# Optimization experiments

Hardware: AMD Instinct MI355X
Metric: run time of the kernel (lower is better)

Reference implementation:

```python
import jax, jax.numpy as jnp
import numpy as np

RES = 14
N = RES * RES
NH = 8
KD = 32
D = 128   # attn_ratio * key_dim
DH = 1024 # D * NH
DIM = 384
B = 128
SCALE = KD ** -0.5


def _bias_idxs():
    pts = [(i, j) for i in range(RES) for j in range(RES)]
    offs, idxs = {}, []
    for p1 in pts:
        for p2 in pts:
            o = (abs(p1[0] - p2[0]), abs(p1[1] - p2[1]))
            offs.setdefault(o, len(offs))
            idxs.append(offs[o])
    return np.array(idxs, np.int32).reshape(N, N), len(offs)

BIAS_IDXS, NUM_OFF = _bias_idxs()  # (N, N), 196 distinct |offset| pairs


def setup_inputs() -> dict:
    key = jax.random.key(0)
    ks = jax.random.split(key, 32)
    g = lambda i, shape, s=0.05: jax.random.normal(ks[i], shape, jnp.float32) * s
    pos = lambda i, shape: jax.random.uniform(ks[i], shape, jnp.float32, minval=0.5, maxval=1.5)
    return dict(
        x=jax.random.normal(ks[0], (B, DIM, RES, RES), jnp.float32),
        qw=g(1, (NH * KD, DIM)), qb=g(2, (NH * KD,)), q_s=pos(3, (NH * KD,)), q_t=g(4, (NH * KD,)),
        kw=g(5, (NH * KD, DIM)), kb=g(6, (NH * KD,)), k_s=pos(7, (NH * KD,)), k_t=g(8, (NH * KD,)),
        vw=g(9, (DH, DIM)), vb=g(10, (DH,)), v_s=pos(11, (DH,)), v_t=g(12, (DH,)),
        lvw=g(13, (DH, 3, 3)), lvb=g(14, (DH,)), lv_s=pos(15, (DH,)), lv_t=g(16, (DH,)),
        th1w=g(17, (NH, NH), 0.3), th1b=g(18, (NH,)),
        th2w=g(19, (NH, NH), 0.3), th2b=g(20, (NH,)),
        ab=g(21, (NH, NUM_OFF)),
        pw=g(22, (DIM, DH)), pb=g(23, (DIM,)), p_s=pos(24, (DIM,)), p_t=g(25, (DIM,)),
    )


def _c(v):
    return v[None, :, None, None]


def conv1x1_bn(x, w, b, s, t):
    # 1x1 conv (NCHW) + eval-mode BN folded to per-channel affine
    y = jnp.einsum('bchw,oc->bohw', x, w) + _c(b)
    return y * _c(s) + _c(t)


def reference(x, qw, qb, q_s, q_t, kw, kb, k_s, k_t, vw, vb, v_s, v_t,
              lvw, lvb, lv_s, lv_t, th1w, th1b, th2w, th2b, ab,
              pw, pb, p_s, p_t):
    Bb = x.shape[0]
    # q,k: (B, NH, N, KD)
    q = conv1x1_bn(x, qw, qb, q_s, q_t).reshape(Bb, NH, KD, N).transpose(0, 1, 3, 2)
    k = conv1x1_bn(x, kw, kb, k_s, k_t).reshape(Bb, NH, KD, N).transpose(0, 1, 3, 2)
    v4 = conv1x1_bn(x, vw, vb, v_s, v_t)  # (B, DH, RES, RES)
    # local depthwise 3x3 conv + BN on v
    vl = jax.lax.conv_general_dilated(
        v4, lvw.reshape(DH, 1, 3, 3), window_strides=(1, 1), padding='SAME',
        dimension_numbers=('NCHW', 'OIHW', 'NCHW'), feature_group_count=DH)
    vl = (vl + _c(lvb)) * _c(lv_s) + _c(lv_t)
    v = v4.reshape(Bb, NH, D, N).transpose(0, 1, 3, 2)  # (B, NH, N, D)

    attn = jnp.einsum('bhid,bhjd->bhij', q, k) * SCALE
    attn = attn + ab[:, BIAS_IDXS][None]  # relative-position bias (1, NH, N, N)
    attn = jnp.einsum('bhij,gh->bgij', attn, th1w) + _c(th1b)  # talking head 1
    attn = jax.nn.softmax(attn, axis=-1)
    attn = jnp.einsum('bhij,gh->bgij', attn, th2w) + _c(th2b)  # talking head 2

    o = jnp.einsum('bhij,bhjd->bhid', attn, v)  # (B, NH, N, D)
    o = o.transpose(0, 1, 3, 2).reshape(Bb, DH, RES, RES) + vl
    o = jax.nn.relu(o)
    return conv1x1_bn(o, pw, pb, p_s, p_t)
```

## Files before the change

### kernel.cpp

```cpp
#include <hip/hip_runtime.h>
#include <hip/hip_bf16.h>
#include <stdint.h>

typedef __hip_bfloat16 bf16;
typedef short short4v __attribute__((ext_vector_type(4)));
typedef short short8 __attribute__((ext_vector_type(8)));
typedef float f32x4 __attribute__((ext_vector_type(4)));
typedef float f32x16 __attribute__((ext_vector_type(16)));

#define NB 128
#define NPIX 196
#define NPAD 208
#define VP 208
#define QROWS 208
#define NH 8
#define KD 32
#define DHEAD 128
#define DH 1024
#define DIM 384
#define SCALE 0.17677669529663687f

__device__ __forceinline__ float b2f(bf16 v) { return __bfloat162float(v); }
__device__ __forceinline__ bf16 f2b(float f) { return __float2bfloat16(f); }
__device__ __forceinline__ float us2f(unsigned short u) {
  union { unsigned int i; float f; } v; v.i = (unsigned int)u << 16; return v.f;
}
__device__ __forceinline__ short f2us(float f) {
  bf16 b = __float2bfloat16(f);
  return *(short*)&b;
}

__device__ __forceinline__ void gll16(const void* g, void* l) {
  auto gp = reinterpret_cast<const uint32_t __attribute__((address_space(1)))*>(
      reinterpret_cast<uintptr_t>(g));
  auto lp = reinterpret_cast<uint32_t __attribute__((address_space(3)))*>(
      reinterpret_cast<uintptr_t>(l));
  __builtin_amdgcn_global_load_lds(gp, lp, 16, 0, 0);
}

__global__ __launch_bounds__(256) void k_cvt4(const float* __restrict__ s0,
                                              const float* __restrict__ s1,
                                              const float* __restrict__ s2,
                                              const float* __restrict__ s3,
                                              bf16* __restrict__ dst,
                                              const float* __restrict__ th1w,
                                              const float* __restrict__ th1b,
                                              const float* __restrict__ ab,
                                              float* __restrict__ ab2g,
                                              float* __restrict__ c1g) {
  if (blockIdx.x >= 3840) {
    int t = threadIdx.x;
    for (int pos = t; pos < NH * NPIX; pos += 256) {
      int g = pos / NPIX, off = pos - g * NPIX;
      float s = th1b[g];
#pragma unroll
      for (int h = 0; h < 8; ++h)
        s += th1w[g * 8 + h] * ab[h * NPIX + off];
      ab2g[pos] = s;
    }
    if (t < 64) c1g[t] = th1w[t] * SCALE;
    return;
  }
  int i = blockIdx.x * 256 + threadIdx.x;
  const float* src; int o;
  if (i < 98304)       { src = s0; o = i; }
  else if (i < 196608) { src = s1; o = i - 98304; }
  else if (i < 589824) { src = s2; o = i - 196608; }
  else                 { src = s3; o = i - 589824; }
  dst[i] = f2b(src[o]);
}

__global__ __launch_bounds__(256) void k_xt(const float* __restrict__ x,
                                            bf16* __restrict__ XT) {
  __shared__ bf16 tile[32][33];
  int ct = blockIdx.x, nt = blockIdx.y, b = blockIdx.z;
  int c0 = ct * 32, n0 = nt * 32;
  int tc = threadIdx.x >> 5, tn = threadIdx.x & 31;
#pragma unroll
  for (int r = 0; r < 4; ++r) {
    int c = tc + r * 8;
    int n = n0 + tn;
    float v = 0.f;
    if (n < NPIX) v = x[((size_t)b * DIM + c0 + c) * NPIX + n];
    tile[c][tn] = f2b(v);
  }
  __syncthreads();
#pragma unroll
  for (int r = 0; r < 4; ++r) {
    int n = n0 + tc + r * 8;
    if (n < NPAD) XT[((size_t)b * NPAD + n) * DIM + c0 + tn] = tile[tn][tc + r * 8];
  }
}

__global__ __launch_bounds__(256, 2) void k_qkv2(
    const bf16* __restrict__ Wf, const bf16* __restrict__ XT,
    const float* __restrict__ qb, const float* __restrict__ qs, const float* __restrict__ qt,
    const float* __restrict__ kb, const float* __restrict__ ks, const float* __restrict__ kt,
    const float* __restrict__ vb, const float* __restrict__ vs, const float* __restrict__ vt,
    bf16* __restrict__ qf, bf16* __restrict__ kf, bf16* __restrict__ v4) {
  __shared__ __align__(16) char lds[2][32768];
  const int NWG = 12 * 208;
  int id = blockIdx.x;
  int id2 = (id & 7) * (NWG >> 3) + (id >> 3);
  int mt = id2 % 12, nt = id2 / 12;
  int m0 = mt * 128, n0 = nt * 128;
  int tid = threadIdx.x, lane = tid & 63;
  int wv = tid >> 6, wm = wv >> 1, wn = wv & 1;

  f32x4 acc[4][4];
#pragma unroll
  for (int mi = 0; mi < 4; ++mi)
#pragma unroll
    for (int ni = 0; ni < 4; ++ni)
#pragma unroll
      for (int r = 0; r < 4; ++r) acc[mi][ni][r] = 0.f;

  auto stage = [&](int buf, int t) {
    int k0 = t * 64;
#pragma unroll
    for (int j = 0; j < 4; ++j) {
      int gi = tid + j * 256;
      int row = gi >> 3, g = gi & 7;
      int sk = k0 + ((g ^ (row & 7)) << 3);
      gll16(Wf + (size_t)(m0 + row) * DIM + sk, &lds[buf][gi * 16]);
      gll16(XT + (size_t)(n0 + row) * DIM + sk, &lds[buf][16384 + gi * 16]);
    }
  };
  auto compute = [&](int buf) {
    const char* Ab = lds[buf];
    const char* Bb = lds[buf] + 16384;
    int kq = lane >> 4, il = lane & 15;
#pragma unroll
    for (int ksb = 0; ksb < 2; ++ksb) {
      int G = ksb * 4 + kq;
      short8 af[4], bfr[4];
#pragma unroll
      for (int mi = 0; mi < 4; ++mi) {
        int row = wm * 64 + mi * 16 + il;
        af[mi] = *(const short8*)(Ab + row * 128 + ((G ^ (row & 7)) << 4));
      }
#pragma unroll
      for (int ni = 0; ni < 4; ++ni) {
        int row = wn * 64 + ni * 16 + il;
        bfr[ni] = *(const short8*)(Bb + row * 128 + ((G ^ (row & 7)) << 4));
      }
#pragma unroll
      for (int mi = 0; mi < 4; ++mi)
#pragma unroll
        for (int ni = 0; ni < 4; ++ni)
          acc[mi][ni] = __builtin_amdgcn_mfma_f32_16x16x32_bf16(af[mi], bfr[ni], acc[mi][ni], 0, 0, 0);
    }
  };

  stage(0, 0);
  __syncthreads();
  for (int t = 0; t < 6; ++t) {
    if (t < 5) stage((t + 1) & 1, t + 1);
    compute(t & 1);
    __syncthreads();
  }

  int cq = lane >> 4, cn = lane & 15;
#pragma unroll
  for (int mi = 0; mi < 4; ++mi) {
    int mbase = m0 + wm * 64 + mi * 16;
    const float *bp, *sp, *tp;
    int segbase, segid;
    if (mbase < 256)      { bp = qb; sp = qs; tp = qt; segbase = 0;   segid = 0; }
    else if (mbase < 512) { bp = kb; sp = ks; tp = kt; segbase = 256; segid = 1; }
    else                  { bp = vb; sp = vs; tp = vt; segbase = 512; segid = 2; }
#pragma unroll
    for (int r = 0; r < 4; ++r) {
      int ms = mbase - segbase + cq * 4 + r;
      float bi = bp[ms], sc = sp[ms], tt = tp[ms];
#pragma unroll
      for (int ni = 0; ni < 4; ++ni) {
        int n = n0 + wn * 64 + ni * 16 + cn;
        int b = n / NPAD;
        int nn = n - b * NPAD;
        float y = (acc[mi][ni][r] + bi) * sc + tt;
        y = (nn < NPIX) ? y : 0.f;
        if (segid == 2) {
          v4[((size_t)b * DH + ms) * VP + nn] = f2b(y);
        } else {
          bf16* dst = segid ? kf : qf;
          dst[(((size_t)b * NH + (ms >> 5)) * QROWS + nn) * KD + (ms & 31)] = f2b(y);
        }
      }
    }
  }
}

__global__ __launch_bounds__(256, 2) void k_p2(
    const bf16* __restrict__ Pw, const bf16* __restrict__ OT,
    const float* __restrict__ pb, const float* __restrict__ ps, const float* __restrict__ pt,
    float* __restrict__ out) {
  __shared__ __align__(16) char lds[2][32768];
  const int NWG = 3 * 208;
  int id = blockIdx.x;
  int id2 = (id & 7) * (NWG >> 3) + (id >> 3);
  int mt = id2 % 3, nt = id2 / 3;
  int m0 = mt * 128, n0 = nt * 128;
  int tid = threadIdx.x, lane = tid & 63;
  int wv = tid >> 6, wm = wv >> 1, wn = wv & 1;

  f32x4 acc[4][4];
#pragma unroll
  for (int mi = 0; mi < 4; ++mi)
#pragma unroll
    for (int ni = 0; ni < 4; ++ni)
#pragma unroll
      for (int r = 0; r < 4; ++r) acc[mi][ni][r] = 0.f;

  auto stage = [&](int buf, int t) {
    int k0 = t * 64;
#pragma unroll
    for (int j = 0; j < 4; ++j) {
      int gi = tid + j * 256;
      int row = gi >> 3, g = gi & 7;
      int sk = k0 + ((g ^ (row & 7)) << 3);
      gll16(Pw + (size_t)(m0 + row) * DH + sk, &lds[buf][gi * 16]);
      gll16(OT + (size_t)(n0 + row) * DH + sk, &lds[buf][16384 + gi * 16]);
    }
  };
  auto compute = [&](int buf) {
    const char* Ab = lds[buf];
    const char* Bb = lds[buf] + 16384;
    int kq = lane >> 4, il = lane & 15;
#pragma unroll
    for (int ksb = 0; ksb < 2; ++ksb) {
      int G = ksb * 4 + kq;
      short8 af[4], bfr[4];
#pragma unroll
      for (int mi = 0; mi < 4; ++mi) {
        int row = wm * 64 + mi * 16 + il;
        af[mi] = *(const short8*)(Ab + row * 128 + ((G ^ (row & 7)) << 4));
      }
#pragma unroll
      for (int ni = 0; ni < 4; ++ni) {
        int row = wn * 64 + ni * 16 + il;
        bfr[ni] = *(const short8*)(Bb + row * 128 + ((G ^ (row & 7)) << 4));
      }
#pragma unroll
      for (int mi = 0; mi < 4; ++mi)
#pragma unroll
        for (int ni = 0; ni < 4; ++ni)
          acc[mi][ni] = __builtin_amdgcn_mfma_f32_16x16x32_bf16(af[mi], bfr[ni], acc[mi][ni], 0, 0, 0);
    }
  };

  stage(0, 0);
  __syncthreads();
  for (int t = 0; t < 16; ++t) {
    if (t < 15) stage((t + 1) & 1, t + 1);
    compute(t & 1);
    __syncthreads();
  }

  int cq = lane >> 4, cn = lane & 15;
#pragma unroll
  for (int mi = 0; mi < 4; ++mi) {
#pragma unroll
    for (int r = 0; r < 4; ++r) {
      int m = m0 + wm * 64 + mi * 16 + cq * 4 + r;
      float bi = pb[m], sc = ps[m], tt = pt[m];
#pragma unroll
      for (int ni = 0; ni < 4; ++ni) {
        int n = n0 + wn * 64 + ni * 16 + cn;
        int b = n / NPAD;
        int nn = n - b * NPAD;
        if (nn < NPIX)
          out[((size_t)b * DIM + m) * NPIX + nn] = (acc[mi][ni][r] + bi) * sc + tt;
      }
    }
  }
}

__global__ __launch_bounds__(256) void k_dwv(
    const bf16* __restrict__ v4, const float* __restrict__ lvw,
    const float* __restrict__ lvb, const float* __restrict__ lvs,
    const float* __restrict__ lvt, bf16* __restrict__ vl,
    float* __restrict__ vcs) {
  int blk = blockIdx.x;
  int b = blk >> 8, cg = blk & 255;
  int lc = threadIdx.x >> 6, px = threadIdx.x & 63;
  int ch = cg * 4 + lc;
  const bf16* src = v4 + ((size_t)b * DH + ch) * VP;
  float w[9];
#pragma unroll
  for (int i = 0; i < 9; ++i) w[i] = lvw[ch * 9 + i];
  float bb = lvb[ch], ss = lvs[ch], tt = lvt[ch];
  bf16* dst = vl + ((size_t)b * DH + ch) * NPIX;
  float csum = 0.f;
  for (int p = px; p < NPIX; p += 64) {
    int ri = p / 14, ci = p - ri * 14;
    float s = 0.f;
#pragma unroll
    for (int dy = -1; dy <= 1; ++dy)
#pragma unroll
      for (int dx = -1; dx <= 1; ++dx) {
        int rr = ri + dy, cc = ci + dx;
        if (rr >= 0 && rr < 14 && cc >= 0 && cc < 14)
          s += w[(dy + 1) * 3 + dx + 1] * b2f(src[rr * 14 + cc]);
      }
    csum += b2f(src[p]);
    dst[p] = f2b((s + bb) * ss + tt);
  }
  csum += __shfl_xor(csum, 1);
  csum += __shfl_xor(csum, 2);
  csum += __shfl_xor(csum, 4);
  csum += __shfl_xor(csum, 8);
  csum += __shfl_xor(csum, 16);
  csum += __shfl_xor(csum, 32);
  if (px == 0) vcs[b * DH + ch] = csum;
}

#define SROW 448
__device__ __forceinline__ int saddr(int g, int i, int j) {
  int r = j * 2 + ((i & 7) << 4);
  if (r >= SROW) r -= SROW;
  return (g * 16 + i) * SROW + r;
}

__global__ __launch_bounds__(512, 4) void k_att(
    const bf16* __restrict__ qf, const bf16* __restrict__ kf,
    const bf16* __restrict__ v4, const bf16* __restrict__ vl,
    const float* __restrict__ vcs,
    const float* __restrict__ ab2g, const float* __restrict__ c1g,
    const float* __restrict__ th2w, const float* __restrict__ th2b,
    bf16* __restrict__ OT) {
  __shared__ __align__(16) char smem[NH * 16 * SROW];
  __shared__ float smInv[NH * 16];
  int id = blockIdx.x;
  int xcd = id & 7;
  int rest = id >> 3;
  int qt = rest % 13;
  int b = (rest / 13) * 8 + xcd;
  int i0 = qt * 16;
  int tid = threadIdx.x;
  int wave = tid >> 6, lane = tid & 63;
  int il = lane & 15, kh = lane >> 4;

  {
    const bf16* qp = qf + ((size_t)b * NH + wave) * QROWS * KD;
    const bf16* kp = kf + ((size_t)b * NH + wave) * QROWS * KD;
    short8 a = *(const short8*)(qp + (i0 + il) * KD + kh * 8);
    for (int jt = 0; jt < 13; ++jt) {
      short8 bb = *(const short8*)(kp + (jt * 16 + il) * KD + kh * 8);
      f32x4 acc = {0.f, 0.f, 0.f, 0.f};
      acc = __builtin_amdgcn_mfma_f32_16x16x32_bf16(a, bb, acc, 0, 0, 0);
      int j = jt * 16 + il;
#pragma unroll
      for (int r = 0; r < 4; ++r)
        *(bf16*)(smem + saddr(wave, kh * 4 + r, j)) = f2b(acc[r]);
    }
  }
  __syncthreads();
  for (int pos = tid; pos < 16 * NPIX; pos += 512) {
    int i = pos / NPIX, j = pos - i * NPIX;
    float sv[8];
#pragma unroll
    for (int h = 0; h < 8; ++h) sv[h] = b2f(*(const bf16*)(smem + saddr(h, i, j)));
    int ia = i0 + i; if (ia > 195) ia = 195;
    int ri = ia / 14, ci = ia - ri * 14;
    int rj = j / 14, cj = j - rj * 14;
    int dr = ri > rj ? ri - rj : rj - ri;
    int dc = ci > cj ? ci - cj : cj - ci;
    int off = dr * 14 + dc;
    float outv[8];
#pragma unroll
    for (int g = 0; g < 8; ++g) {
      float s = ab2g[g * NPIX + off];
#pragma unroll
      for (int h = 0; h < 8; ++h) s += c1g[g * 8 + h] * sv[h];
      outv[g] = s;
    }
#pragma unroll
    for (int g = 0; g < 8; ++g)
      *(bf16*)(smem + saddr(g, i, j)) = f2b(outv[g]);
  }
  __syncthreads();
  {
    int row = tid >> 2, part = tid & 3;
    int g = row >> 4, i = row & 15;
    int jb = part * 52;
    int n4 = (part == 3) ? 10 : 13;
    float m = -1e30f;
    for (int it = 0; it < n4; ++it) {
      short4v v = *(const short4v*)(smem + saddr(g, i, jb + it * 4));
#pragma unroll
      for (int t = 0; t < 4; ++t) m = fmaxf(m, us2f((unsigned short)v[t]));
    }
    m = fmaxf(m, __shfl_xor(m, 1));
    m = fmaxf(m, __shfl_xor(m, 2));
    float s = 0.f;
    for (int it = 0; it < n4; ++it) {
      char* p = smem + saddr(g, i, jb + it * 4);
      short4v v = *(const short4v*)p;
      short4v w;
#pragma unroll
      for (int t = 0; t < 4; ++t) {
        float e = __expf(us2f((unsigned short)v[t]) - m);
        s += e;
        w[t] = f2us(e);
      }
      *(short4v*)p = w;
    }
    if (part == 3) {
      short4v z = {0, 0, 0, 0};
#pragma unroll
      for (int it = 0; it < 3; ++it)
        *(short4v*)(smem + saddr(g, i, 196 + it * 4)) = z;
    }
    s += __shfl_xor(s, 1);
    s += __shfl_xor(s, 2);
    if (part == 0) smInv[row] = 1.f / s;
  }
  __syncthreads();
  for (int pos = tid; pos < 16 * NPIX; pos += 512) {
    int i = pos / NPIX, j = pos - i * NPIX;
    float pv[8];
#pragma unroll
    for (int g = 0; g < 8; ++g)
      pv[g] = b2f(*(const bf16*)(smem + saddr(g, i, j))) * smInv[g * 16 + i];
#pragma unroll
    for (int g2 = 0; g2 < 8; ++g2) {
      float s = 0.f;
#pragma unroll
      for (int g = 0; g < 8; ++g) s += th2w[g2 * 8 + g] * pv[g];
      *(bf16*)(smem + saddr(g2, i, j)) = f2b(s);
    }
  }
  __syncthreads();
  {
    int g = wave;
    int cl = lane & 31, s = lane >> 5;
    const bf16* vb0 = v4 + ((size_t)b * DH + g * DHEAD) * VP;
    float t2b = th2b[g];
#pragma unroll
    for (int dt2 = 0; dt2 < 4; ++dt2) {
      f32x16 acc;
#pragma unroll
      for (int r = 0; r < 16; ++r) acc[r] = 0.f;
      const bf16* vrow = vb0 + (size_t)(dt2 * 32 + cl) * VP + s * 8;
      for (int ks = 0; ks < 13; ++ks) {
        short8 pa = *(const short8*)(smem + saddr(g, cl & 15, ks * 16 + s * 8));
        short8 av = *(const short8*)(vrow + ks * 16);
        acc = __builtin_amdgcn_mfma_f32_32x32x16_bf16(pa, av, acc, 0, 0, 0);
      }
      int ch = g * DHEAD + dt2 * 32 + cl;
      float csv = vcs[b * DH + ch] * t2b;
      const bf16* vlrow = vl + ((size_t)b * DH + ch) * NPIX;
      bf16* otcol = OT + (size_t)b * NPAD * DH + ch;
#pragma unroll
      for (int reg = 0; reg < 8; ++reg) {
        int i = (reg & 3) + 8 * (reg >> 2) + 4 * s;
        int n = i0 + i;
        if (n < NPIX) {
          float val = acc[reg] + csv + b2f(vlrow[n]);
          otcol[(size_t)n * DH] = f2b(fmaxf(val, 0.f));
        } else {
          otcol[(size_t)n * DH] = f2b(0.f);
        }
      }
    }
  }
}

extern "C" void kernel_launch(void* const* d_in, const int* in_sizes, int n_in,
                              void* d_out, int out_size, void* d_ws, size_t ws_size,
                              hipStream_t stream) {
  const float* x    = (const float*)d_in[0];
  const float* qw   = (const float*)d_in[1];
  const float* qb   = (const float*)d_in[2];
  const float* q_s  = (const float*)d_in[3];
  const float* q_t  = (const float*)d_in[4];
  const float* kw   = (const float*)d_in[5];
  const float* kb   = (const float*)d_in[6];
  const float* k_s  = (const float*)d_in[7];
  const float* k_t  = (const float*)d_in[8];
  const float* vw   = (const float*)d_in[9];
  const float* vb   = (const float*)d_in[10];
  const float* v_s  = (const float*)d_in[11];
  const float* v_t  = (const float*)d_in[12];
  const float* lvw  = (const float*)d_in[13];
  const float* lvb  = (const float*)d_in[14];
  const float* lv_s = (const float*)d_in[15];
  const float* lv_t = (const float*)d_in[16];
  const float* th1w = (const float*)d_in[17];
  const float* th1b = (const float*)d_in[18];
  const float* th2w = (const float*)d_in[19];
  const float* th2b = (const float*)d_in[20];
  const float* ab   = (const float*)d_in[21];
  const float* pw   = (const float*)d_in[22];
  const float* pb   = (const float*)d_in[23];
  const float* p_s  = (const float*)d_in[24];
  const float* p_t  = (const float*)d_in[25];

  char* ws = (char*)d_ws;
  size_t off = 0;
  auto alloc = [&](size_t bytes) {
    char* p = ws + off;
    off += (bytes + 255) & ~(size_t)255;
    return p;
  };
  char* region0 = alloc((size_t)NB * NPAD * DH * 2);
  bf16* XT  = (bf16*)region0;
  bf16* OT  = (bf16*)region0;
  bf16* qfb = (bf16*)alloc((size_t)NB * NH * QROWS * KD * 2);
  bf16* kfb = (bf16*)alloc((size_t)NB * NH * QROWS * KD * 2);
  bf16* v4  = (bf16*)alloc((size_t)NB * DH * VP * 2);
  bf16* vlb = (bf16*)alloc((size_t)NB * DH * NPIX * 2);
  float* vcs = (float*)alloc((size_t)NB * DH * 4);
  bf16* wf  = (bf16*)alloc((size_t)1536 * DIM * 2);
  bf16* wpb = (bf16*)alloc((size_t)DIM * DH * 2);
  float* ab2g = (float*)alloc((size_t)NH * NPIX * 4);
  float* c1g  = (float*)alloc((size_t)64 * 4);
  (void)ws_size; (void)in_sizes; (void)n_in; (void)out_size;

  k_cvt4<<<dim3(3841), 256, 0, stream>>>(qw, kw, vw, pw, wf, th1w, th1b, ab,
                                         ab2g, c1g);
  k_xt<<<dim3(12, 7, NB), 256, 0, stream>>>(x, XT);
  k_qkv2<<<dim3(2496), 256, 0, stream>>>(wf, XT, qb, q_s, q_t, kb, k_s, k_t,
                                         vb, v_s, v_t, qfb, kfb, v4);
  k_dwv<<<dim3(NB * 256), 256, 0, stream>>>(v4, lvw, lvb, lv_s, lv_t, vlb, vcs);
  k_att<<<dim3(1664), 512, 0, stream>>>(qfb, kfb, v4, vlb, vcs,
                                        ab2g, c1g, th2w, th2b, OT);
  k_p2<<<dim3(624), 256, 0, stream>>>(wpb, OT, pb, p_s, p_t, (float*)d_out);
}
```

Before: 419.8 us.

## Fuse talking-head-1 mixing into QK MFMA loop, split key tiles across waves

Each wave now computes QK^T scores for all 8 heads on its own subset of key tiles, keeping the accumulators in registers. It applies the relative-position bias and the talking-head-1 mixing directly before writing to shared memory. This removes one shared-memory round trip, one barrier and the separate mixing pass. In exchange the load is uneven: 13 tiles over 8 waves leaves some waves with two tiles, and register pressure rises from holding 8 q fragments and 8 accumulators.

```diff
diff --git a/kernel.cpp b/kernel.cpp
--- a/kernel.cpp
+++ b/kernel.cpp
@@ -342,42 +342,44 @@
   int il = lane & 15, kh = lane >> 4;
 
   {
-    const bf16* qp = qf + ((size_t)b * NH + wave) * QROWS * KD;
-    const bf16* kp = kf + ((size_t)b * NH + wave) * QROWS * KD;
-    short8 a = *(const short8*)(qp + (i0 + il) * KD + kh * 8);
-    for (int jt = 0; jt < 13; ++jt) {
-      short8 bb = *(const short8*)(kp + (jt * 16 + il) * KD + kh * 8);
-      f32x4 acc = {0.f, 0.f, 0.f, 0.f};
-      acc = __builtin_amdgcn_mfma_f32_16x16x32_bf16(a, bb, acc, 0, 0, 0);
+    const bf16* qp0 = qf + (size_t)b * NH * QROWS * KD + (size_t)(i0 + il) * KD + kh * 8;
+    const bf16* kp0 = kf + (size_t)b * NH * QROWS * KD + (size_t)il * KD + kh * 8;
+    short8 aq[8];
+#pragma unroll
+    for (int g = 0; g < 8; ++g)
+      aq[g] = *(const short8*)(qp0 + (size_t)g * QROWS * KD);
+    int ri4[4], ci4[4];
+#pragma unroll
+    for (int r = 0; r < 4; ++r) {
+      int ia = i0 + kh * 4 + r; if (ia > 195) ia = 195;
+      int rr = ia / 14;
+      ri4[r] = rr; ci4[r] = ia - rr * 14;
+    }
+    for (int jt = wave; jt < 13; jt += 8) {
+      f32x4 acc[8];
+#pragma unroll
+      for (int g = 0; g < 8; ++g) {
+        short8 bb = *(const short8*)(kp0 + (size_t)g * QROWS * KD + jt * 16 * KD);
+        f32x4 z = {0.f, 0.f, 0.f, 0.f};
+        acc[g] = __builtin_amdgcn_mfma_f32_16x16x32_bf16(aq[g], bb, z, 0, 0, 0);
+      }
       int j = jt * 16 + il;
-#pragma unroll
-      for (int r = 0; r < 4; ++r)
-        *(bf16*)(smem + saddr(wave, kh * 4 + r, j)) = f2b(acc[r]);
-    }
-  }
-  __syncthreads();
-  for (int pos = tid; pos < 16 * NPIX; pos += 512) {
-    int i = pos / NPIX, j = pos - i * NPIX;
-    float sv[8];
-#pragma unroll
-    for (int h = 0; h < 8; ++h) sv[h] = b2f(*(const bf16*)(smem + saddr(h, i, j)));
-    int ia = i0 + i; if (ia > 195) ia = 195;
-    int ri = ia / 14, ci = ia - ri * 14;
-    int rj = j / 14, cj = j - rj * 14;
-    int dr = ri > rj ? ri - rj : rj - ri;
-    int dc = ci > cj ? ci - cj : cj - ci;
-    int off = dr * 14 + dc;
-    float outv[8];
-#pragma unroll
-    for (int g = 0; g < 8; ++g) {
-      float s = ab2g[g * NPIX + off];
-#pragma unroll
-      for (int h = 0; h < 8; ++h) s += c1g[g * 8 + h] * sv[h];
-      outv[g] = s;
-    }
-#pragma unroll
-    for (int g = 0; g < 8; ++g)
-      *(bf16*)(smem + saddr(g, i, j)) = f2b(outv[g]);
+      int jc = j > 195 ? 195 : j;
+      int rj = jc / 14, cj = jc - rj * 14;
+#pragma unroll
+      for (int r = 0; r < 4; ++r) {
+        int dr = ri4[r] > rj ? ri4[r] - rj : rj - ri4[r];
+        int dc = ci4[r] > cj ? ci4[r] - cj : cj - ci4[r];
+        int off = dr * 14 + dc;
+#pragma unroll
+        for (int g2 = 0; g2 < 8; ++g2) {
+          float s = ab2g[g2 * NPIX + off];
+#pragma unroll
+          for (int g = 0; g < 8; ++g) s += c1g[g2 * 8 + g] * acc[g][r];
+          *(bf16*)(smem + saddr(g2, kh * 4 + r, j)) = f2b(s);
+        }
+      }
+    }
   }
   __syncthreads();
   {
```

Result: slower. 456.6 us (+8.8%).
